# Kernel tuning notes

Measured on AMD Instinct MI355X. Metric: run time of the kernel, lower is better.

Reference implementation:

```python
import jax, jax.numpy as jnp
import numpy as np
import math

B, S, E, H = 1, 4096, 1024, 16
D = E // H  # head_dim = 64

def setup_inputs() -> dict:
    key = jax.random.key(0)
    kx, kq, kk, kv, ko = jax.random.split(key, 5)
    sc = 1.0 / math.sqrt(E)
    return {
        "x": jax.random.normal(kx, (B, S, E), dtype=jnp.float32),
        "Wq": jax.random.normal(kq, (E, E), dtype=jnp.float32) * sc,
        "Wk": jax.random.normal(kk, (E, E), dtype=jnp.float32) * sc,
        "Wv": jax.random.normal(kv, (E, E), dtype=jnp.float32) * sc,
        "Wo": jax.random.normal(ko, (E, E), dtype=jnp.float32) * sc,
    }

def reference(x, Wq, Wk, Wv, Wo):
    b, s, _ = x.shape
    # nn.Linear(no bias): x @ W.T ; then split heads -> [b, H, s, D]
    def heads(w):
        return (x @ w.T).reshape(b, s, H, D).transpose(0, 2, 1, 3)
    q, k, v = heads(Wq), heads(Wk), heads(Wv)
    scale = 1.0 / math.sqrt(D)
    logits = jnp.einsum('bhqd,bhkd->bhqk', q, k) * scale  # [b,H,s,s]
    causal = jnp.tril(jnp.ones((s, s), dtype=bool))
    logits = jnp.where(causal, logits, -jnp.inf)
    attn = jax.nn.softmax(logits, axis=-1)
    out = jnp.einsum('bhqk,bhkd->bhqd', attn, v)  # [b,H,s,D]
    out = out.transpose(0, 2, 1, 3).reshape(b, s, E)
    return out @ Wo.T
```

## Files before the change

### kernel.cpp

```cpp
#include <hip/hip_runtime.h>
#include <hip/hip_bf16.h>

typedef unsigned short u16;
typedef unsigned int u32;
typedef __attribute__((ext_vector_type(8))) short short8;
typedef __attribute__((ext_vector_type(4))) float f32x4;
typedef __attribute__((ext_vector_type(16))) float f32x16;
typedef __attribute__((ext_vector_type(4))) u32 u32x4;
typedef __attribute__((ext_vector_type(2))) u32 u32x2;


__device__ __forceinline__ u16 f2b(float f) {
  unsigned u = __float_as_uint(f);
  u = (u + 0x7FFFu + ((u >> 16) & 1u)) >> 16;
  return (u16)u;
}

__device__ __forceinline__ u32 pkbf(float lo, float hi) {
  __hip_bfloat162 b = __float22bfloat162_rn(make_float2(lo, hi));
  u32 r;
  __builtin_memcpy(&r, &b, 4);
  return r;
}

__device__ __forceinline__ u32x2 plswap(u32 a, u32 b) {
  return __builtin_amdgcn_permlane32_swap(a, b, false, false);
}

__device__ __forceinline__ void gload16(const void* g, void* l) {
  __builtin_amdgcn_global_load_lds(
      (const __attribute__((address_space(1))) void*)g,
      (__attribute__((address_space(3))) void*)l, 16, 0, 0);
}


__global__ __launch_bounds__(256) void f2bf_kernel(const float* __restrict__ in,
                                                   u16* __restrict__ out, int n,
                                                   float scale) {
  int i = (blockIdx.x * 256 + threadIdx.x) * 4;
  if (i >= n) return;
  float4 v = *(const float4*)(in + i);
  unsigned p0 = (unsigned)f2b(v.x * scale) | ((unsigned)f2b(v.y * scale) << 16);
  unsigned p1 = (unsigned)f2b(v.z * scale) | ((unsigned)f2b(v.w * scale) << 16);
  *(uint2*)(out + i) = make_uint2(p0, p1);
}


__global__ __launch_bounds__(256) void transpose_kernel(const u16* __restrict__ V,
                                                        u16* __restrict__ Vt) {
  __shared__ u16 t[32][33];
  int bx = blockIdx.x;
  int by = blockIdx.y;
  int c = threadIdx.x & 31, r4 = threadIdx.x >> 5;
#pragma unroll
  for (int i = 0; i < 4; ++i) {
    int row = r4 * 4 + i;
    t[row][c] = V[(size_t)(by * 32 + row) * 1024 + bx * 32 + c];
  }
  __syncthreads();
#pragma unroll
  for (int i = 0; i < 4; ++i) {
    int row = r4 * 4 + i;
    Vt[(size_t)(bx * 32 + row) * 4096 + by * 32 + c] = t[c][row];
  }
}


__device__ __forceinline__ void storeC(u16* C, size_t idx, float v) { C[idx] = f2b(v); }
__device__ __forceinline__ void storeC(float* C, size_t idx, float v) { C[idx] = v; }

template <typename OutT>
__device__ __forceinline__ void gemm_body(const u16* __restrict__ A,
                                          const u16* __restrict__ B,
                                          OutT* __restrict__ C) {
  __shared__ __align__(16) u16 lA[128 * 32];
  __shared__ __align__(16) u16 lB[128 * 32];
  const int tid = threadIdx.x;
  const int w = tid >> 6, lane = tid & 63, g = lane >> 4, lr = lane & 15;
  const int wr = w >> 1, wc = w & 1;
  const int m0 = blockIdx.y * 128, n0 = blockIdx.x * 128;

  f32x4 acc[4][4] = {};

  for (int k0 = 0; k0 < 1024; k0 += 32) {
#pragma unroll
    for (int j = 0; j < 2; ++j) {
      int c = tid + j * 256;
      gload16(A + (size_t)(m0 + (c >> 2)) * 1024 + k0 + (c & 3) * 8,
              &lA[(j * 256 + w * 64) * 8]);
      gload16(B + (size_t)(n0 + (c >> 2)) * 1024 + k0 + (c & 3) * 8,
              &lB[(j * 256 + w * 64) * 8]);
    }
    __syncthreads();

    short8 af[4], bf[4];
#pragma unroll
    for (int i = 0; i < 4; ++i) {
      af[i] = *(const short8*)&lA[(wr * 64 + i * 16 + lr) * 32 + g * 8];
      bf[i] = *(const short8*)&lB[(wc * 64 + i * 16 + lr) * 32 + g * 8];
    }
#pragma unroll
    for (int mi = 0; mi < 4; ++mi)
#pragma unroll
      for (int ni = 0; ni < 4; ++ni)
        acc[mi][ni] =
            __builtin_amdgcn_mfma_f32_16x16x32_bf16(af[mi], bf[ni], acc[mi][ni], 0, 0, 0);
    __syncthreads();
  }

#pragma unroll
  for (int mi = 0; mi < 4; ++mi)
#pragma unroll
    for (int ni = 0; ni < 4; ++ni)
#pragma unroll
      for (int r = 0; r < 4; ++r) {
        size_t row = (size_t)(m0 + wr * 64 + mi * 16 + g * 4 + r);
        size_t col = (size_t)(n0 + wc * 64 + ni * 16 + lr);
        storeC(C, row * 1024 + col, acc[mi][ni][r]);
      }
}

__global__ __launch_bounds__(256) void gemm_qkv_kernel(
    const u16* __restrict__ A, const u16* __restrict__ W0, const u16* __restrict__ W1,
    const u16* __restrict__ W2, u16* __restrict__ C0, u16* __restrict__ C1,
    u16* __restrict__ C2) {
  int z = blockIdx.z;
  const u16* B = (z == 0) ? W0 : (z == 1) ? W1 : W2;
  u16* C = (z == 0) ? C0 : (z == 1) ? C1 : C2;
  gemm_body<u16>(A, B, C);
}

__global__ __launch_bounds__(256) void gemm_out_kernel(const u16* __restrict__ A,
                                                       const u16* __restrict__ B,
                                                       float* __restrict__ C) {
  gemm_body<float>(A, B, C);
}


#define NEGINF (-30000.0f)

__global__ __launch_bounds__(512, 4) void attn_kernel(const u16* __restrict__ Qg,
                                                      const u16* __restrict__ Kg,
                                                      const u16* __restrict__ Vtg,
                                                      u16* __restrict__ Og) {
  __shared__ __align__(16) char smem[65536];
  __shared__ float lll[4][32];

  const int tid = threadIdx.x, lane = tid & 63;
  const int w8 = tid >> 6, p = w8 >> 2, qw = w8 & 3;
  const int l31 = lane & 31, hi = lane >> 5;
  const int bid = blockIdx.x;
  const int h = bid & 15;
  const int i32 = bid >> 4;
  const int qb = (i32 < 16) ? (31 - i32) : (i32 - 16);
  const int qs = qb * 128;
  const int qsw = qs + qw * 32;
  const int iters = qb + 1;
  const int kstart = p ? iters : 0;
  const int dtw = qsw >> 6;
  const int swz = (l31 & 7) << 4;

  const u32x4 onesu = {0x3F803F80u, 0x3F803F80u, 0x3F803F80u, 0x3F803F80u};
  const short8 ones = __builtin_bit_cast(short8, onesu);

  short8 qf[4];
  {
    const u16* Qp = Qg + (size_t)(qsw + l31) * 1024 + h * 64 + hi * 8;
#pragma unroll
    for (int kc = 0; kc < 4; ++kc) qf[kc] = *(const short8*)(Qp + kc * 16);
  }

  const int j0 = qw * 2;
  auto stage = [&](int b, int kt) {
    char* Kb = smem + (((p << 1) | b) << 14);
    char* Vb = Kb + 8192;
#pragma unroll
    for (int jj = 0; jj < 2; ++jj) {
      const int j = j0 + jj;
      const int row = (j << 3) + (lane >> 3);
      const int c = (lane & 7) ^ (row & 7);
      gload16(Kg + (size_t)(kt * 64 + row) * 1024 + h * 64 + c * 8,
              Kb + (j << 10));
      gload16(Vtg + (size_t)(h * 64 + row) * 4096 + kt * 64 + c * 8,
              Vb + (j << 10));
    }
  };

  f32x16 ot[2] = {};
  f32x16 lacc = {};

  int cur = 0;
  stage(0, kstart);
  __syncthreads();

  for (int it = 0; it < iters; ++it) {
    const int kt = kstart + it;
    if (it + 1 < iters) stage(cur ^ 1, kt + 1);

    const bool doCompute = (p == 0) || (kt <= dtw);
    if (doCompute) {
      const char* Kb = smem + (((p << 1) | cur) << 14);
      const char* Vb = Kb + 8192;

      f32x16 st0 = {}, st1 = {};
#pragma unroll
      for (int kc = 0; kc < 4; ++kc) {
        short8 k0 = *(const short8*)(Kb + l31 * 128 + ((((kc << 1) | hi) << 4) ^ swz));
        st0 = __builtin_amdgcn_mfma_f32_32x32x16_bf16(k0, qf[kc], st0, 0, 0, 0);
      }
#pragma unroll
      for (int kc = 0; kc < 4; ++kc) {
        short8 k1 =
            *(const short8*)(Kb + 4096 + l31 * 128 + ((((kc << 1) | hi) << 4) ^ swz));
        st1 = __builtin_amdgcn_mfma_f32_32x32x16_bf16(k1, qf[kc], st1, 0, 0, 0);
      }

      if (kt == dtw) {
        const int q = qsw + l31;
#pragma unroll
        for (int r = 0; r < 16; ++r) {
          int key = kt * 64 + (r & 3) + 8 * (r >> 2) + 4 * hi;
          if (key > q) st0[r] = NEGINF;
          if (key + 32 > q) st1[r] = NEGINF;
        }
      }

#pragma unroll
      for (int r = 0; r < 16; ++r) {
        st0[r] = __builtin_amdgcn_exp2f(st0[r] - 12.f);
        st1[r] = __builtin_amdgcn_exp2f(st1[r] - 12.f);
      }

#pragma unroll
      for (int kt2 = 0; kt2 < 2; ++kt2) {
        const f32x16& st = kt2 ? st1 : st0;
        short8 pa[2];
#pragma unroll
        for (int ks = 0; ks < 2; ++ks) {
          const int b = 8 * ks;
          u32 pk0 = pkbf(st[b + 0], st[b + 1]);
          u32 pk1 = pkbf(st[b + 2], st[b + 3]);
          u32 pk2 = pkbf(st[b + 4], st[b + 5]);
          u32 pk3 = pkbf(st[b + 6], st[b + 7]);
          u32x2 r02 = plswap(pk0, pk2);
          u32x2 r13 = plswap(pk1, pk3);
          u32x4 t;
          t.x = r02.x;
          t.y = r13.x;
          t.z = r02.y;
          t.w = r13.y;
          pa[ks] = __builtin_bit_cast(short8, t);
        }
        lacc = __builtin_amdgcn_mfma_f32_32x32x16_bf16(ones, pa[0], lacc, 0, 0, 0);
        lacc = __builtin_amdgcn_mfma_f32_32x32x16_bf16(ones, pa[1], lacc, 0, 0, 0);
#pragma unroll
        for (int dt = 0; dt < 2; ++dt)
#pragma unroll
          for (int ks = 0; ks < 2; ++ks) {
            short8 vfv = *(const short8*)(Vb + dt * 4096 + l31 * 128 +
                                          (((kt2 * 4 + ks * 2 + hi) << 4) ^ swz));
            ot[dt] =
                __builtin_amdgcn_mfma_f32_32x32x16_bf16(vfv, pa[ks], ot[dt], 0, 0, 0);
          }
      }
    }
    __syncthreads();
    cur ^= 1;
  }

  __syncthreads();
  float* lOfw = (float*)smem + (qw << 11);
  char* pw = smem + 32768 + (qw << 12);
  if (p == 0) {
#pragma unroll
    for (int dt = 0; dt < 2; ++dt)
#pragma unroll
      for (int r = 0; r < 16; ++r) {
        int d = dt * 32 + (r & 3) + 8 * (r >> 2) + 4 * hi;
        lOfw[d * 32 + l31] = ot[dt][r];
      }
    if (hi == 0) lll[qw][l31] = lacc[0];
  }
  __syncthreads();
  if (p == 1) {
    float inv = 1.0f / (lll[qw][l31] + lacc[0]);
#pragma unroll
    for (int dt = 0; dt < 2; ++dt)
#pragma unroll
      for (int r = 0; r < 16; ++r) {
        int d = dt * 32 + (r & 3) + 8 * (r >> 2) + 4 * hi;
        float val = (lOfw[d * 32 + l31] + ot[dt][r]) * inv;
        *(u16*)(pw + l31 * 128 + ((d * 2) ^ ((l31 & 7) << 4))) = f2b(val);
      }
  }
  __syncthreads();
  if (p == 1) {
    const int row = lane >> 1;
#pragma unroll
    for (int ii = 0; ii < 4; ++ii) {
      int c = (lane & 1) * 4 + ii;
      short8 v = *(const short8*)(pw + row * 128 + ((c * 16) ^ ((row & 7) << 4)));
      *(short8*)(Og + (size_t)(qsw + row) * 1024 + h * 64 + c * 8) = v;
    }
  }
}


extern "C" void kernel_launch(void* const* d_in, const int* in_sizes, int n_in,
                              void* d_out, int out_size, void* d_ws, size_t ws_size,
                              hipStream_t stream) {
  const float* x = (const float*)d_in[0];
  const float* Wq = (const float*)d_in[1];
  const float* Wk = (const float*)d_in[2];
  const float* Wv = (const float*)d_in[3];
  const float* Wo = (const float*)d_in[4];
  float* out = (float*)d_out;
  char* ws = (char*)d_ws;
  const size_t MB = 1024 * 1024;

  u16* xb  = (u16*)(ws);
  u16* wqb = (u16*)(ws + 8 * MB);
  u16* wkb = (u16*)(ws + 10 * MB);
  u16* wvb = (u16*)(ws + 12 * MB);
  u16* wob = (u16*)(ws + 14 * MB);
  u16* Qb  = (u16*)(ws + 16 * MB);
  u16* Kb  = (u16*)(ws + 24 * MB);
  u16* Vb  = (u16*)(ws + 32 * MB);
  u16* Vtb = (u16*)(ws + 40 * MB);
  u16* att = xb;

  const float qscale = 0.125f * 1.4426950408889634f;

  f2bf_kernel<<<4096, 256, 0, stream>>>(x, xb, 4096 * 1024, 1.f);
  f2bf_kernel<<<1024, 256, 0, stream>>>(Wq, wqb, 1024 * 1024, qscale);
  f2bf_kernel<<<1024, 256, 0, stream>>>(Wk, wkb, 1024 * 1024, 1.f);
  f2bf_kernel<<<1024, 256, 0, stream>>>(Wv, wvb, 1024 * 1024, 1.f);
  f2bf_kernel<<<1024, 256, 0, stream>>>(Wo, wob, 1024 * 1024, 1.f);

  gemm_qkv_kernel<<<dim3(8, 32, 3), 256, 0, stream>>>(xb, wqb, wkb, wvb, Qb, Kb, Vb);
  transpose_kernel<<<dim3(32, 128), 256, 0, stream>>>(Vb, Vtb);
  attn_kernel<<<512, 512, 0, stream>>>(Qb, Kb, Vtb, att);
  gemm_out_kernel<<<dim3(8, 32), 256, 0, stream>>>(att, wob, out);
}
```

Before: 147.6 us.

## Deepen GEMM K-tile with swizzled LDS, narrow output-GEMM tile, batch weight casts

The GEMM K-step grows from 32 to 64 and LDS rows get an XOR swizzle, which halves the barrier count and aims to remove bank conflicts on fragment reads. The output projection switches to 64-wide N tiles, doubling its grid so more CUs are busy. The four weight conversions become one launch, cutting launch overhead. The cost is more LDS per block and slightly more complex addressing.

```diff
diff --git a/kernel.cpp b/kernel.cpp
--- a/kernel.cpp
+++ b/kernel.cpp
@@ -45,6 +45,22 @@
   *(uint2*)(out + i) = make_uint2(p0, p1);
 }
 
+__global__ __launch_bounds__(256) void f2bf4_kernel(
+    const float* __restrict__ w0, const float* __restrict__ w1,
+    const float* __restrict__ w2, const float* __restrict__ w3,
+    u16* __restrict__ o0, u16* __restrict__ o1, u16* __restrict__ o2,
+    u16* __restrict__ o3, float scale0) {
+  const int y = blockIdx.y;
+  const float* in = (y == 0) ? w0 : (y == 1) ? w1 : (y == 2) ? w2 : w3;
+  u16* out = (y == 0) ? o0 : (y == 1) ? o1 : (y == 2) ? o2 : o3;
+  const float scale = (y == 0) ? scale0 : 1.f;
+  int i = (blockIdx.x * 256 + threadIdx.x) * 4;
+  float4 v = *(const float4*)(in + i);
+  unsigned p0 = (unsigned)f2b(v.x * scale) | ((unsigned)f2b(v.y * scale) << 16);
+  unsigned p1 = (unsigned)f2b(v.z * scale) | ((unsigned)f2b(v.w * scale) << 16);
+  *(uint2*)(out + i) = make_uint2(p0, p1);
+}
+
 
 __global__ __launch_bounds__(256) void transpose_kernel(const u16* __restrict__ V,
                                                         u16* __restrict__ Vt) {
@@ -69,53 +85,65 @@
 __device__ __forceinline__ void storeC(u16* C, size_t idx, float v) { C[idx] = f2b(v); }
 __device__ __forceinline__ void storeC(float* C, size_t idx, float v) { C[idx] = v; }
 
-template <typename OutT>
+template <int BN, typename OutT>
 __device__ __forceinline__ void gemm_body(const u16* __restrict__ A,
                                           const u16* __restrict__ B,
                                           OutT* __restrict__ C) {
-  __shared__ __align__(16) u16 lA[128 * 32];
-  __shared__ __align__(16) u16 lB[128 * 32];
+  constexpr int NF = BN / 32;
+  constexpr int BJ = BN / 32;
+  __shared__ __align__(16) u16 lA[128 * 64];
+  __shared__ __align__(16) u16 lB[BN * 64];
   const int tid = threadIdx.x;
   const int w = tid >> 6, lane = tid & 63, g = lane >> 4, lr = lane & 15;
   const int wr = w >> 1, wc = w & 1;
-  const int m0 = blockIdx.y * 128, n0 = blockIdx.x * 128;
-
-  f32x4 acc[4][4] = {};
-
-  for (int k0 = 0; k0 < 1024; k0 += 32) {
-#pragma unroll
-    for (int j = 0; j < 2; ++j) {
+  const int m0 = blockIdx.y * 128, n0 = blockIdx.x * BN;
+
+  f32x4 acc[4][NF] = {};
+
+  for (int k0 = 0; k0 < 1024; k0 += 64) {
+#pragma unroll
+    for (int j = 0; j < 4; ++j) {
       int c = tid + j * 256;
-      gload16(A + (size_t)(m0 + (c >> 2)) * 1024 + k0 + (c & 3) * 8,
+      int row = c >> 3, sub = (c & 7) ^ (row & 7);
+      gload16(A + (size_t)(m0 + row) * 1024 + k0 + sub * 8,
               &lA[(j * 256 + w * 64) * 8]);
-      gload16(B + (size_t)(n0 + (c >> 2)) * 1024 + k0 + (c & 3) * 8,
-              &lB[(j * 256 + w * 64) * 8]);
+      if (j < BJ)
+        gload16(B + (size_t)(n0 + row) * 1024 + k0 + sub * 8,
+                &lB[(j * 256 + w * 64) * 8]);
     }
     __syncthreads();
 
-    short8 af[4], bf[4];
-#pragma unroll
-    for (int i = 0; i < 4; ++i) {
-      af[i] = *(const short8*)&lA[(wr * 64 + i * 16 + lr) * 32 + g * 8];
-      bf[i] = *(const short8*)&lB[(wc * 64 + i * 16 + lr) * 32 + g * 8];
-    }
-#pragma unroll
-    for (int mi = 0; mi < 4; ++mi)
-#pragma unroll
-      for (int ni = 0; ni < 4; ++ni)
-        acc[mi][ni] =
-            __builtin_amdgcn_mfma_f32_16x16x32_bf16(af[mi], bf[ni], acc[mi][ni], 0, 0, 0);
+#pragma unroll
+    for (int k2 = 0; k2 < 2; ++k2) {
+      short8 af[4], bf[NF];
+#pragma unroll
+      for (int i = 0; i < 4; ++i) {
+        int row = wr * 64 + i * 16 + lr;
+        af[i] = *(const short8*)&lA[row * 64 + ((((k2 << 2) | g) ^ (row & 7)) << 3)];
+      }
+#pragma unroll
+      for (int i = 0; i < NF; ++i) {
+        int row = wc * (BN / 2) + i * 16 + lr;
+        bf[i] = *(const short8*)&lB[row * 64 + ((((k2 << 2) | g) ^ (row & 7)) << 3)];
+      }
+#pragma unroll
+      for (int mi = 0; mi < 4; ++mi)
+#pragma unroll
+        for (int ni = 0; ni < NF; ++ni)
+          acc[mi][ni] = __builtin_amdgcn_mfma_f32_16x16x32_bf16(af[mi], bf[ni],
+                                                                acc[mi][ni], 0, 0, 0);
+    }
     __syncthreads();
   }
 
 #pragma unroll
   for (int mi = 0; mi < 4; ++mi)
 #pragma unroll
-    for (int ni = 0; ni < 4; ++ni)
+    for (int ni = 0; ni < NF; ++ni)
 #pragma unroll
       for (int r = 0; r < 4; ++r) {
         size_t row = (size_t)(m0 + wr * 64 + mi * 16 + g * 4 + r);
-        size_t col = (size_t)(n0 + wc * 64 + ni * 16 + lr);
+        size_t col = (size_t)(n0 + wc * (BN / 2) + ni * 16 + lr);
         storeC(C, row * 1024 + col, acc[mi][ni][r]);
       }
 }
@@ -127,13 +155,13 @@
   int z = blockIdx.z;
   const u16* B = (z == 0) ? W0 : (z == 1) ? W1 : W2;
   u16* C = (z == 0) ? C0 : (z == 1) ? C1 : C2;
-  gemm_body<u16>(A, B, C);
+  gemm_body<128, u16>(A, B, C);
 }
 
 __global__ __launch_bounds__(256) void gemm_out_kernel(const u16* __restrict__ A,
                                                        const u16* __restrict__ B,
                                                        float* __restrict__ C) {
-  gemm_body<float>(A, B, C);
+  gemm_body<64, float>(A, B, C);
 }
 
 
@@ -332,13 +360,11 @@
   const float qscale = 0.125f * 1.4426950408889634f;
 
   f2bf_kernel<<<4096, 256, 0, stream>>>(x, xb, 4096 * 1024, 1.f);
-  f2bf_kernel<<<1024, 256, 0, stream>>>(Wq, wqb, 1024 * 1024, qscale);
-  f2bf_kernel<<<1024, 256, 0, stream>>>(Wk, wkb, 1024 * 1024, 1.f);
-  f2bf_kernel<<<1024, 256, 0, stream>>>(Wv, wvb, 1024 * 1024, 1.f);
-  f2bf_kernel<<<1024, 256, 0, stream>>>(Wo, wob, 1024 * 1024, 1.f);
+  f2bf4_kernel<<<dim3(1024, 4), 256, 0, stream>>>(Wq, Wk, Wv, Wo, wqb, wkb, wvb,
+                                                  wob, qscale);
 
   gemm_qkv_kernel<<<dim3(8, 32, 3), 256, 0, stream>>>(xb, wqb, wkb, wvb, Qb, Kb, Vb);
   transpose_kernel<<<dim3(32, 128), 256, 0, stream>>>(Vb, Vtb);
   attn_kernel<<<512, 512, 0, stream>>>(Qb, Kb, Vtb, att);
-  gemm_out_kernel<<<dim3(8, 32), 256, 0, stream>>>(att, wob, out);
-}
+  gemm_out_kernel<<<dim3(16, 32), 256, 0, stream>>>(att, wob, out);
+}
```

Result: faster. 134.0 us (-9.2%).
